# Performance work log

Hardware: AMD Instinct MI355X
Metric: run time of the kernel (lower is better)

Reference implementation:

```python
import jax, jax.numpy as jnp
import numpy as np

B, T, D, TY = 64, 512, 96, 512
H, DK = 4, 32            # num_heads, embed_dim_per_head
E = H * DK               # embed_dim = 128
P = 2                    # function='L' -> 2 coefficients
L, HID = 64, 128         # latent_dim, hidden_dim


def setup_inputs() -> dict:
    key = jax.random.key(0)
    ks = jax.random.split(key, 16)
    inp = {
        "timesteps": jax.random.uniform(ks[0], (B, T), jnp.float32),
        "X": jax.random.normal(ks[1], (B, T, D), jnp.float32),
        "M": jax.random.randint(ks[2], (B, T, D), 0, 2).astype(jnp.float32),
        "y_time_steps": jax.random.uniform(ks[3], (B, TY), jnp.float32),
        # time_embedding: Linear(1, E)
        "te_w": jax.random.normal(ks[4], (E,), jnp.float32),
        "te_b": jax.random.normal(ks[5], (E,), jnp.float32) * 0.1,
        # learned query [1, P, E]
        "query": jax.random.normal(ks[6], (1, P, E), jnp.float32),
        # query_map / key_map: Linear(E, E), stored [in, out]
        "q_w": jax.random.normal(ks[7], (E, E), jnp.float32) / np.sqrt(E),
        "q_b": jax.random.normal(ks[8], (E,), jnp.float32) * 0.1,
        "k_w": jax.random.normal(ks[9], (E, E), jnp.float32) / np.sqrt(E),
        "k_b": jax.random.normal(ks[10], (E,), jnp.float32) * 0.1,
        # attn shared out: Linear(2D*H, L)
        "ow": jax.random.normal(ks[11], (2 * D * H, L), jnp.float32) / np.sqrt(2 * D * H),
        "ob": jnp.zeros((L,), jnp.float32),
        # decoder MLP: Linear(L,HID)+ReLU+Linear(HID,D)
        "w1": jax.random.normal(ks[12], (L, HID), jnp.float32) / np.sqrt(L),
        "b1": jnp.zeros((HID,), jnp.float32),
        "w2": jax.random.normal(ks[13], (HID, D), jnp.float32) / np.sqrt(HID),
        "b2": jnp.zeros((D,), jnp.float32),
    }
    return inp


def _fld_forward(timesteps, X, M, y_time_steps, te_w, te_b, query,
                 q_w, q_b, k_w, k_b, ow, ob, w1, b1, w2, b2):
    b, t, d = X.shape
    # time embedding: Linear(1,E), sin applied to indices i % H == 0
    emb = timesteps[..., None] * te_w + te_b               # [B,T,E]
    sin_idx = (jnp.arange(E) % H) == 0
    emb = jnp.where(sin_idx, jnp.sin(emb), emb)

    X_cat = jnp.concatenate([X, M], axis=-1)               # [B,T,2D]
    M_cat = jnp.concatenate([M, M], axis=-1)               # [B,T,2D]

    q = query @ q_w + q_b                                   # [1,P,E]
    k = emb @ k_w + k_b                                     # [B,T,E]
    q = q.reshape(1, P, H, DK).transpose(0, 2, 1, 3)        # [1,H,P,dk]
    k = k.reshape(b, t, H, DK).transpose(0, 2, 1, 3)        # [B,H,T,dk]

    scores = jnp.einsum('xhpd,bhtd->bhpt', q, k) / np.sqrt(DK)  # [B,H,P,T]
    # broadcast over value feature dim, mask per-feature, softmax over T
    logits = jnp.where(M_cat[:, None, None, :, :] == 0, -jnp.inf,
                       scores[..., None])                   # [B,H,P,T,2D]
    p = jax.nn.softmax(logits, axis=-2)
    xa = jnp.einsum('bhptf,btf->bhpf', p, X_cat)            # [B,H,P,2D]
    xa = xa.transpose(0, 2, 1, 3).reshape(b, P, H * 2 * d)  # [B,P,H*2D]
    coeffs = xa @ ow + ob                                   # [B,P,L]

    # function 'L': linear in y_time_steps
    x = coeffs[:, 0][:, None, :] + y_time_steps[:, :, None] * coeffs[:, 1][:, None, :]
    h1 = jax.nn.relu(x @ w1 + b1)
    return h1 @ w2 + b2                                     # [B,TY,D]


def reference(timesteps, X, M, y_time_steps, te_w, te_b, query,
              q_w, q_b, k_w, k_b, ow, ob, w1, b1, w2, b2):
    return _fld_forward(timesteps, X, M, y_time_steps, te_w, te_b, query,
                        q_w, q_b, k_w, k_b, ow, ob, w1, b1, w2, b2)
```

## Files before the change

### kernel.cpp

```cpp
#include <hip/hip_runtime.h>
#include <math.h>

#define B_   64
#define T_   512
#define D_   96
#define TY_  512
#define H_   4
#define DK_  32
#define E_   128
#define P_   2
#define L_   64
#define HID_ 128

#define WS_OB2P  1024
#define WS_PN    2048
#define WS_PD    395264
#define WS_AB    788480

__global__ __launch_bounds__(256) void kspool(
    const float* __restrict__ tsteps, const float* __restrict__ te_w,
    const float* __restrict__ te_b,   const float* __restrict__ X,
    const float* __restrict__ M,      const float* __restrict__ query,
    const float* __restrict__ q_w,    const float* __restrict__ q_b,
    const float* __restrict__ k_w,    const float* __restrict__ k_b,
    const float* __restrict__ ow,     float* __restrict__ ws)
{
    const int c = blockIdx.x, b = blockIdx.y, tid = threadIdx.x;
    __shared__ float qm[P_ * E_];
    __shared__ float w2q_s[E_ * 8];
    __shared__ float tw_s[E_], tb_s[E_], bq_s[8];
    __shared__ float w_s[64 * 8];
    __shared__ float red[96 * 17];
    __shared__ float obp2[4][64];

    {
        int p = tid >> 7, ep = tid & 127;
        float acc = q_b[ep];
        #pragma unroll 4
        for (int e = 0; e < E_; ++e)
            acc += query[p * E_ + e] * q_w[e * E_ + ep];
        qm[p * E_ + ep] = acc;
    }
    if (tid < E_) { tw_s[tid] = te_w[tid]; tb_s[tid] = te_b[tid]; }
    __syncthreads();
    const float rs = 0.17677669529663687f;
    #pragma unroll
    for (int i = 0; i < 4; ++i) {
        int idx = tid + i * 256;
        int e = idx >> 3, hp = idx & 7, h = hp >> 1, p = hp & 1;
        float acc = 0.f;
        #pragma unroll
        for (int dk = 0; dk < DK_; ++dk)
            acc += k_w[e * E_ + h * DK_ + dk] * qm[p * E_ + h * DK_ + dk];
        w2q_s[idx] = acc * rs;
    }
    if (tid < 8) {
        int hp = tid, h = hp >> 1, p = hp & 1;
        float acc = 0.f;
        #pragma unroll
        for (int dk = 0; dk < DK_; ++dk)
            acc += k_b[h * DK_ + dk] * qm[p * E_ + h * DK_ + dk];
        bq_s[hp] = acc * rs;
    }
    __syncthreads();

    {
        const int t = tid & 63, hpg = tid >> 6, hp0 = hpg * 2;
        const float tv = tsteps[b * T_ + c * 64 + t];
        float a0 = 0.f, a1 = 0.f;
        #pragma unroll 4
        for (int e = 0; e < E_; ++e) {
            float v = tv * tw_s[e] + tb_s[e];
            if ((e & 3) == 0) v = __sinf(v);
            float2 w = *(const float2*)&w2q_s[e * 8 + hp0];
            a0 += v * w.x;
            a1 += v * w.y;
        }
        w_s[t * 8 + hp0]     = __expf(a0 + bq_s[hp0]);
        w_s[t * 8 + hp0 + 1] = __expf(a1 + bq_s[hp0 + 1]);
    }
    __syncthreads();

    const int fid = tid & 127, slice = tid >> 7;
    float num[8] = {0.f, 0.f, 0.f, 0.f, 0.f, 0.f, 0.f, 0.f};
    float den[8] = {0.f, 0.f, 0.f, 0.f, 0.f, 0.f, 0.f, 0.f};
    if (fid < 96) {
        #pragma unroll 4
        for (int i = 0; i < 32; ++i) {
            int tl = slice + 2 * i;
            size_t base = ((size_t)(b * T_ + c * 64 + tl)) * D_ + fid;
            float m = M[base], x = X[base];
            float mx = m * x;
            const float* wr = w_s + tl * 8;
            #pragma unroll
            for (int hp = 0; hp < 8; ++hp) {
                num[hp] += wr[hp] * mx;
                den[hp] += wr[hp] * m;
            }
        }
    }
    __syncthreads();
    if (slice == 1 && fid < 96) {
        #pragma unroll
        for (int hp = 0; hp < 8; ++hp) {
            red[fid * 17 + hp]     = num[hp];
            red[fid * 17 + 8 + hp] = den[hp];
        }
    }
    __syncthreads();
    if (slice == 0 && fid < 96) {
        float* pN = ws + WS_PN + ((size_t)((b * 8 + c) * 8)) * 96;
        float* pD = ws + WS_PD + ((size_t)((b * 8 + c) * 8)) * 96;
        #pragma unroll
        for (int hp = 0; hp < 8; ++hp) {
            pN[hp * 96 + fid] = num[hp] + red[fid * 17 + hp];
            pD[hp * 96 + fid] = den[hp] + red[fid * 17 + 8 + hp];
        }
    }

    if (b == 0) {
        int sub = tid >> 6, l = tid & 63;
        float acc = 0.f;
        #pragma unroll
        for (int k = 0; k < 12; ++k) {
            int hj = c * 48 + sub * 12 + k;
            int h = hj / 96, j = hj - h * 96;
            acc += ow[(size_t)(h * 2 * D_ + D_ + j) * L_ + l];
        }
        obp2[sub][l] = acc;
        __syncthreads();
        if (sub == 0)
            ws[WS_OB2P + c * 64 + l] = obp2[0][l] + obp2[1][l] + obp2[2][l] + obp2[3][l];
    }
}

__global__ __launch_bounds__(256) void kab(
    const float* __restrict__ ow, const float* __restrict__ w1,
    const float* __restrict__ b1, const float* __restrict__ ob,
    float* __restrict__ ws)
{
    const int b = blockIdx.x, tid = threadIdx.x;
    __shared__ float xa_s[8 * 96];
    __shared__ float cfp[4][2][64];
    __shared__ float cf_s[2][64];
    __shared__ float abp[2][2][128];

    for (int flat = tid; flat < 8 * 96; flat += 256) {
        int hp = flat / 96, f = flat - hp * 96;
        float n = 0.f, d = 0.f;
        #pragma unroll
        for (int c = 0; c < 8; ++c) {
            n += ws[WS_PN + ((size_t)((b * 8 + c) * 8 + hp)) * 96 + f];
            d += ws[WS_PD + ((size_t)((b * 8 + c) * 8 + hp)) * 96 + f];
        }
        xa_s[flat] = n / d;
    }
    __syncthreads();

    #pragma unroll
    for (int it = 0; it < 2; ++it) {
        int idx = tid + it * 256;
        int h = idx >> 7, p = (idx >> 6) & 1, l = idx & 63;
        const float* xr = xa_s + (h * 2 + p) * 96;
        const float* owr = ow + (size_t)(h * 2 * D_) * L_ + l;
        float acc = 0.f;
        #pragma unroll 4
        for (int f = 0; f < 96; ++f)
            acc += xr[f] * owr[(size_t)f * L_];
        cfp[h][p][l] = acc;
    }
    __syncthreads();

    if (tid < 128) {
        int p = tid >> 6, l = tid & 63;
        float v = cfp[0][p][l] + cfp[1][p][l] + cfp[2][p][l] + cfp[3][p][l] + ob[l];
        #pragma unroll
        for (int g = 0; g < 8; ++g) v += ws[WS_OB2P + g * 64 + l];
        cf_s[p][l] = v;
    }
    __syncthreads();

    {
        int s = tid >> 7, j = tid & 127;
        float a0 = 0.f, a1 = 0.f;
        #pragma unroll 4
        for (int li = 0; li < 32; ++li) {
            int l = s * 32 + li;
            float wv = w1[l * HID_ + j];
            a0 += cf_s[0][l] * wv;
            a1 += cf_s[1][l] * wv;
        }
        abp[s][0][j] = a0;
        abp[s][1][j] = a1;
    }
    __syncthreads();

    if (tid < 128) {
        ws[WS_AB + b * 256 + tid] = abp[0][0][tid] + abp[1][0][tid] + b1[tid];
    } else {
        int j = tid - 128;
        ws[WS_AB + b * 256 + 128 + j] = abp[0][1][j] + abp[1][1][j];
    }
}

__global__ __launch_bounds__(256) void kdec(
    const float* __restrict__ yts, const float* __restrict__ w2,
    const float* __restrict__ b2,  const float* __restrict__ ws,
    float* __restrict__ out)
{
    __shared__ float w2_s[HID_ * D_];
    __shared__ float a0_s[HID_], a1_s[HID_];
    __shared__ float y_s[64];
    const int tid = threadIdx.x;
    const int posb = blockIdx.x * 64;
    const int b = posb >> 9;

    {
        const float4* src = (const float4*)w2;
        float4* dst = (float4*)w2_s;
        #pragma unroll
        for (int i = 0; i < 12; ++i) dst[tid + i * 256] = src[tid + i * 256];
    }
    if (tid < 64) y_s[tid] = yts[posb + tid];
    if (tid >= 64 && tid < 192) {
        int j = tid - 64;
        a0_s[j] = ws[WS_AB + b * 256 + j];
        a1_s[j] = ws[WS_AB + b * 256 + 128 + j];
    }
    __syncthreads();

    const int pos = tid & 63, ds = tid >> 6;
    const float y = y_s[pos];
    const float* wrow = w2_s + ds * 24;

    float acc[24];
    #pragma unroll
    for (int dd = 0; dd < 24; ++dd) acc[dd] = 0.f;

    #pragma unroll 4
    for (int j = 0; j < HID_; ++j) {
        float h = fmaxf(0.f, a0_s[j] + y * a1_s[j]);
        const float* wr = wrow + j * D_;
        #pragma unroll
        for (int q = 0; q < 6; ++q) {
            float4 w4 = *(const float4*)(wr + q * 4);
            acc[q * 4 + 0] += h * w4.x;
            acc[q * 4 + 1] += h * w4.y;
            acc[q * 4 + 2] += h * w4.z;
            acc[q * 4 + 3] += h * w4.w;
        }
    }

    float* op = out + ((size_t)(posb + pos)) * D_ + ds * 24;
    const float* bp = b2 + ds * 24;
    #pragma unroll
    for (int q = 0; q < 6; ++q) {
        float4 v;
        v.x = acc[q * 4 + 0] + bp[q * 4 + 0];
        v.y = acc[q * 4 + 1] + bp[q * 4 + 1];
        v.z = acc[q * 4 + 2] + bp[q * 4 + 2];
        v.w = acc[q * 4 + 3] + bp[q * 4 + 3];
        *(float4*)(op + q * 4) = v;
    }
}

extern "C" void kernel_launch(void* const* d_in, const int* in_sizes, int n_in,
                              void* d_out, int out_size, void* d_ws, size_t ws_size,
                              hipStream_t stream)
{
    const float* timesteps = (const float*)d_in[0];
    const float* X         = (const float*)d_in[1];
    const float* M         = (const float*)d_in[2];
    const float* yts       = (const float*)d_in[3];
    const float* te_w      = (const float*)d_in[4];
    const float* te_b      = (const float*)d_in[5];
    const float* query     = (const float*)d_in[6];
    const float* q_w       = (const float*)d_in[7];
    const float* q_b       = (const float*)d_in[8];
    const float* k_w       = (const float*)d_in[9];
    const float* k_b       = (const float*)d_in[10];
    const float* ow        = (const float*)d_in[11];
    const float* ob        = (const float*)d_in[12];
    const float* w1        = (const float*)d_in[13];
    const float* b1        = (const float*)d_in[14];
    const float* w2        = (const float*)d_in[15];
    const float* b2        = (const float*)d_in[16];
    float* out = (float*)d_out;
    float* ws  = (float*)d_ws;

    kspool<<<dim3(8, B_), 256, 0, stream>>>(timesteps, te_w, te_b, X, M,
                                            query, q_w, q_b, k_w, k_b, ow, ws);
    kab<<<B_, 256, 0, stream>>>(ow, w1, b1, ob, ws);
    kdec<<<(B_ * TY_) / 64, 256, 0, stream>>>(yts, w2, b2, ws, out);
}
```

Before: 163.1 us.

## Fuse three kernels into one cooperative kernel with grid sync

Merges the pooling, coefficient and decoder kernels into a single cooperative launch of 512 blocks that synchronise across the grid between phases. A union of shared-memory layouts lets both phases reuse the same LDS. The coefficient MLP is now recomputed redundantly in each of the 512 decoder blocks instead of once per batch, and the w2 weight load is issued early into registers to overlap with that work. Falls back to two ordinary launches if the cooperative launch fails. This trades launch overhead and the intermediate round-trip for a grid barrier and duplicated small GEMMs.

```diff
diff --git a/kernel.cpp b/kernel.cpp
--- a/kernel.cpp
+++ b/kernel.cpp
@@ -1,5 +1,8 @@
 #include <hip/hip_runtime.h>
+#include <hip/hip_cooperative_groups.h>
 #include <math.h>
+
+namespace cg = cooperative_groups;
 
 #define B_   64
 #define T_   512
@@ -15,9 +18,31 @@
 #define WS_OB2P  1024
 #define WS_PN    2048
 #define WS_PD    395264
-#define WS_AB    788480
-
-__global__ __launch_bounds__(256) void kspool(
+
+struct SMemP1 {
+    float qm[P_ * E_];
+    float w2q[E_ * 8];
+    float tw[E_], tb[E_], bq[8];
+    float w[64 * 8];
+    float red[96 * 17];
+    float obp2[4][64];
+};
+struct SMemP2 {
+    float w2s[HID_ * D_];
+    float xa[8 * 96];
+    float cfp[4][2][64];
+    float cf[2][64];
+    float a0[HID_], a1[HID_];
+    float ys[64];
+    float abp[2][2][128];
+};
+union SMem {
+    SMemP1 p1;
+    SMemP2 p2;
+};
+
+__device__ __forceinline__ void phase1(
+    SMem& sm, int bi, int tid,
     const float* __restrict__ tsteps, const float* __restrict__ te_w,
     const float* __restrict__ te_b,   const float* __restrict__ X,
     const float* __restrict__ M,      const float* __restrict__ query,
@@ -25,13 +50,8 @@
     const float* __restrict__ k_w,    const float* __restrict__ k_b,
     const float* __restrict__ ow,     float* __restrict__ ws)
 {
-    const int c = blockIdx.x, b = blockIdx.y, tid = threadIdx.x;
-    __shared__ float qm[P_ * E_];
-    __shared__ float w2q_s[E_ * 8];
-    __shared__ float tw_s[E_], tb_s[E_], bq_s[8];
-    __shared__ float w_s[64 * 8];
-    __shared__ float red[96 * 17];
-    __shared__ float obp2[4][64];
+    const int c = bi & 7, b = bi >> 3;
+    SMemP1& p1 = sm.p1;
 
     {
         int p = tid >> 7, ep = tid & 127;
@@ -39,9 +59,9 @@
         #pragma unroll 4
         for (int e = 0; e < E_; ++e)
             acc += query[p * E_ + e] * q_w[e * E_ + ep];
-        qm[p * E_ + ep] = acc;
-    }
-    if (tid < E_) { tw_s[tid] = te_w[tid]; tb_s[tid] = te_b[tid]; }
+        p1.qm[p * E_ + ep] = acc;
+    }
+    if (tid < E_) { p1.tw[tid] = te_w[tid]; p1.tb[tid] = te_b[tid]; }
     __syncthreads();
     const float rs = 0.17677669529663687f;
     #pragma unroll
@@ -51,16 +71,16 @@
         float acc = 0.f;
         #pragma unroll
         for (int dk = 0; dk < DK_; ++dk)
-            acc += k_w[e * E_ + h * DK_ + dk] * qm[p * E_ + h * DK_ + dk];
-        w2q_s[idx] = acc * rs;
+            acc += k_w[e * E_ + h * DK_ + dk] * p1.qm[p * E_ + h * DK_ + dk];
+        p1.w2q[idx] = acc * rs;
     }
     if (tid < 8) {
         int hp = tid, h = hp >> 1, p = hp & 1;
         float acc = 0.f;
         #pragma unroll
         for (int dk = 0; dk < DK_; ++dk)
-            acc += k_b[h * DK_ + dk] * qm[p * E_ + h * DK_ + dk];
-        bq_s[hp] = acc * rs;
+            acc += k_b[h * DK_ + dk] * p1.qm[p * E_ + h * DK_ + dk];
+        p1.bq[hp] = acc * rs;
     }
     __syncthreads();
 
@@ -70,14 +90,14 @@
         float a0 = 0.f, a1 = 0.f;
         #pragma unroll 4
         for (int e = 0; e < E_; ++e) {
-            float v = tv * tw_s[e] + tb_s[e];
+            float v = tv * p1.tw[e] + p1.tb[e];
             if ((e & 3) == 0) v = __sinf(v);
-            float2 w = *(const float2*)&w2q_s[e * 8 + hp0];
+            float2 w = *(const float2*)&p1.w2q[e * 8 + hp0];
             a0 += v * w.x;
             a1 += v * w.y;
         }
-        w_s[t * 8 + hp0]     = __expf(a0 + bq_s[hp0]);
-        w_s[t * 8 + hp0 + 1] = __expf(a1 + bq_s[hp0 + 1]);
+        p1.w[t * 8 + hp0]     = __expf(a0 + p1.bq[hp0]);
+        p1.w[t * 8 + hp0 + 1] = __expf(a1 + p1.bq[hp0 + 1]);
     }
     __syncthreads();
 
@@ -91,7 +111,7 @@
             size_t base = ((size_t)(b * T_ + c * 64 + tl)) * D_ + fid;
             float m = M[base], x = X[base];
             float mx = m * x;
-            const float* wr = w_s + tl * 8;
+            const float* wr = p1.w + tl * 8;
             #pragma unroll
             for (int hp = 0; hp < 8; ++hp) {
                 num[hp] += wr[hp] * mx;
@@ -103,8 +123,8 @@
     if (slice == 1 && fid < 96) {
         #pragma unroll
         for (int hp = 0; hp < 8; ++hp) {
-            red[fid * 17 + hp]     = num[hp];
-            red[fid * 17 + 8 + hp] = den[hp];
+            p1.red[fid * 17 + hp]     = num[hp];
+            p1.red[fid * 17 + 8 + hp] = den[hp];
         }
     }
     __syncthreads();
@@ -113,8 +133,8 @@
         float* pD = ws + WS_PD + ((size_t)((b * 8 + c) * 8)) * 96;
         #pragma unroll
         for (int hp = 0; hp < 8; ++hp) {
-            pN[hp * 96 + fid] = num[hp] + red[fid * 17 + hp];
-            pD[hp * 96 + fid] = den[hp] + red[fid * 17 + 8 + hp];
+            pN[hp * 96 + fid] = num[hp] + p1.red[fid * 17 + hp];
+            pD[hp * 96 + fid] = den[hp] + p1.red[fid * 17 + 8 + hp];
         }
     }
 
@@ -127,33 +147,44 @@
             int h = hj / 96, j = hj - h * 96;
             acc += ow[(size_t)(h * 2 * D_ + D_ + j) * L_ + l];
         }
-        obp2[sub][l] = acc;
+        p1.obp2[sub][l] = acc;
         __syncthreads();
         if (sub == 0)
-            ws[WS_OB2P + c * 64 + l] = obp2[0][l] + obp2[1][l] + obp2[2][l] + obp2[3][l];
-    }
-}
-
-__global__ __launch_bounds__(256) void kab(
-    const float* __restrict__ ow, const float* __restrict__ w1,
-    const float* __restrict__ b1, const float* __restrict__ ob,
-    float* __restrict__ ws)
-{
-    const int b = blockIdx.x, tid = threadIdx.x;
-    __shared__ float xa_s[8 * 96];
-    __shared__ float cfp[4][2][64];
-    __shared__ float cf_s[2][64];
-    __shared__ float abp[2][2][128];
-
-    for (int flat = tid; flat < 8 * 96; flat += 256) {
+            ws[WS_OB2P + c * 64 + l] = p1.obp2[0][l] + p1.obp2[1][l]
+                                     + p1.obp2[2][l] + p1.obp2[3][l];
+    }
+}
+
+__device__ __forceinline__ void phase2(
+    SMem& sm, int bi, int tid,
+    const float* __restrict__ ow, const float* __restrict__ ob,
+    const float* __restrict__ w1, const float* __restrict__ b1,
+    const float* __restrict__ yts, const float* __restrict__ w2,
+    const float* __restrict__ b2, const float* __restrict__ ws,
+    float* __restrict__ out)
+{
+    SMemP2& p2 = sm.p2;
+    const int b = bi >> 3;
+
+    float4 wreg[12];
+    {
+        const float4* src = (const float4*)w2;
+        #pragma unroll
+        for (int i = 0; i < 12; ++i) wreg[i] = src[tid + i * 256];
+    }
+    if (tid < 64) p2.ys[tid] = yts[bi * 64 + tid];
+
+    #pragma unroll
+    for (int it = 0; it < 3; ++it) {
+        int flat = tid + it * 256;
         int hp = flat / 96, f = flat - hp * 96;
         float n = 0.f, d = 0.f;
         #pragma unroll
-        for (int c = 0; c < 8; ++c) {
-            n += ws[WS_PN + ((size_t)((b * 8 + c) * 8 + hp)) * 96 + f];
-            d += ws[WS_PD + ((size_t)((b * 8 + c) * 8 + hp)) * 96 + f];
-        }
-        xa_s[flat] = n / d;
+        for (int cc = 0; cc < 8; ++cc) {
+            n += ws[WS_PN + ((size_t)((b * 8 + cc) * 8 + hp)) * 96 + f];
+            d += ws[WS_PD + ((size_t)((b * 8 + cc) * 8 + hp)) * 96 + f];
+        }
+        p2.xa[flat] = n / d;
     }
     __syncthreads();
 
@@ -161,22 +192,23 @@
     for (int it = 0; it < 2; ++it) {
         int idx = tid + it * 256;
         int h = idx >> 7, p = (idx >> 6) & 1, l = idx & 63;
-        const float* xr = xa_s + (h * 2 + p) * 96;
+        const float* xr = p2.xa + (h * 2 + p) * 96;
         const float* owr = ow + (size_t)(h * 2 * D_) * L_ + l;
         float acc = 0.f;
         #pragma unroll 4
         for (int f = 0; f < 96; ++f)
             acc += xr[f] * owr[(size_t)f * L_];
-        cfp[h][p][l] = acc;
+        p2.cfp[h][p][l] = acc;
     }
     __syncthreads();
 
     if (tid < 128) {
         int p = tid >> 6, l = tid & 63;
-        float v = cfp[0][p][l] + cfp[1][p][l] + cfp[2][p][l] + cfp[3][p][l] + ob[l];
+        float v = p2.cfp[0][p][l] + p2.cfp[1][p][l] + p2.cfp[2][p][l]
+                + p2.cfp[3][p][l] + ob[l];
         #pragma unroll
         for (int g = 0; g < 8; ++g) v += ws[WS_OB2P + g * 64 + l];
-        cf_s[p][l] = v;
+        p2.cf[p][l] = v;
     }
     __syncthreads();
 
@@ -187,51 +219,30 @@
         for (int li = 0; li < 32; ++li) {
             int l = s * 32 + li;
             float wv = w1[l * HID_ + j];
-            a0 += cf_s[0][l] * wv;
-            a1 += cf_s[1][l] * wv;
-        }
-        abp[s][0][j] = a0;
-        abp[s][1][j] = a1;
+            a0 += p2.cf[0][l] * wv;
+            a1 += p2.cf[1][l] * wv;
+        }
+        p2.abp[s][0][j] = a0;
+        p2.abp[s][1][j] = a1;
     }
     __syncthreads();
 
     if (tid < 128) {
-        ws[WS_AB + b * 256 + tid] = abp[0][0][tid] + abp[1][0][tid] + b1[tid];
+        p2.a0[tid] = p2.abp[0][0][tid] + p2.abp[1][0][tid] + b1[tid];
     } else {
         int j = tid - 128;
-        ws[WS_AB + b * 256 + 128 + j] = abp[0][1][j] + abp[1][1][j];
-    }
-}
-
-__global__ __launch_bounds__(256) void kdec(
-    const float* __restrict__ yts, const float* __restrict__ w2,
-    const float* __restrict__ b2,  const float* __restrict__ ws,
-    float* __restrict__ out)
-{
-    __shared__ float w2_s[HID_ * D_];
-    __shared__ float a0_s[HID_], a1_s[HID_];
-    __shared__ float y_s[64];
-    const int tid = threadIdx.x;
-    const int posb = blockIdx.x * 64;
-    const int b = posb >> 9;
-
-    {
-        const float4* src = (const float4*)w2;
-        float4* dst = (float4*)w2_s;
-        #pragma unroll
-        for (int i = 0; i < 12; ++i) dst[tid + i * 256] = src[tid + i * 256];
-    }
-    if (tid < 64) y_s[tid] = yts[posb + tid];
-    if (tid >= 64 && tid < 192) {
-        int j = tid - 64;
-        a0_s[j] = ws[WS_AB + b * 256 + j];
-        a1_s[j] = ws[WS_AB + b * 256 + 128 + j];
+        p2.a1[j] = p2.abp[0][1][j] + p2.abp[1][1][j];
+    }
+    {
+        float4* dst = (float4*)p2.w2s;
+        #pragma unroll
+        for (int i = 0; i < 12; ++i) dst[tid + i * 256] = wreg[i];
     }
     __syncthreads();
 
     const int pos = tid & 63, ds = tid >> 6;
-    const float y = y_s[pos];
-    const float* wrow = w2_s + ds * 24;
+    const float y = p2.ys[pos];
+    const float* wrow = p2.w2s + ds * 24;
 
     float acc[24];
     #pragma unroll
@@ -239,7 +250,7 @@
 
     #pragma unroll 4
     for (int j = 0; j < HID_; ++j) {
-        float h = fmaxf(0.f, a0_s[j] + y * a1_s[j]);
+        float h = fmaxf(0.f, p2.a0[j] + y * p2.a1[j]);
         const float* wr = wrow + j * D_;
         #pragma unroll
         for (int q = 0; q < 6; ++q) {
@@ -251,7 +262,7 @@
         }
     }
 
-    float* op = out + ((size_t)(posb + pos)) * D_ + ds * 24;
+    float* op = out + ((size_t)(bi * 64 + pos)) * D_ + ds * 24;
     const float* bp = b2 + ds * 24;
     #pragma unroll
     for (int q = 0; q < 6; ++q) {
@@ -262,6 +273,51 @@
         v.w = acc[q * 4 + 3] + bp[q * 4 + 3];
         *(float4*)(op + q * 4) = v;
     }
+}
+
+__global__ __launch_bounds__(256) void kfused(
+    const float* __restrict__ tsteps, const float* __restrict__ te_w,
+    const float* __restrict__ te_b,   const float* __restrict__ X,
+    const float* __restrict__ M,      const float* __restrict__ query,
+    const float* __restrict__ q_w,    const float* __restrict__ q_b,
+    const float* __restrict__ k_w,    const float* __restrict__ k_b,
+    const float* __restrict__ ow,     const float* __restrict__ ob,
+    const float* __restrict__ w1,     const float* __restrict__ b1,
+    const float* __restrict__ yts,    const float* __restrict__ w2,
+    const float* __restrict__ b2,     float* __restrict__ ws,
+    float* __restrict__ out)
+{
+    __shared__ SMem sm;
+    const int bi = blockIdx.x, tid = threadIdx.x;
+    phase1(sm, bi, tid, tsteps, te_w, te_b, X, M, query,
+           q_w, q_b, k_w, k_b, ow, ws);
+    __threadfence();
+    cg::this_grid().sync();
+    phase2(sm, bi, tid, ow, ob, w1, b1, yts, w2, b2, ws, out);
+}
+
+__global__ __launch_bounds__(256) void kphase1(
+    const float* __restrict__ tsteps, const float* __restrict__ te_w,
+    const float* __restrict__ te_b,   const float* __restrict__ X,
+    const float* __restrict__ M,      const float* __restrict__ query,
+    const float* __restrict__ q_w,    const float* __restrict__ q_b,
+    const float* __restrict__ k_w,    const float* __restrict__ k_b,
+    const float* __restrict__ ow,     float* __restrict__ ws)
+{
+    __shared__ SMem sm;
+    phase1(sm, blockIdx.x, threadIdx.x, tsteps, te_w, te_b, X, M, query,
+           q_w, q_b, k_w, k_b, ow, ws);
+}
+
+__global__ __launch_bounds__(256) void kphase2(
+    const float* __restrict__ ow, const float* __restrict__ ob,
+    const float* __restrict__ w1, const float* __restrict__ b1,
+    const float* __restrict__ yts, const float* __restrict__ w2,
+    const float* __restrict__ b2, const float* __restrict__ ws,
+    float* __restrict__ out)
+{
+    __shared__ SMem sm;
+    phase2(sm, blockIdx.x, threadIdx.x, ow, ob, w1, b1, yts, w2, b2, ws, out);
 }
 
 extern "C" void kernel_launch(void* const* d_in, const int* in_sizes, int n_in,
@@ -288,8 +344,19 @@
     float* out = (float*)d_out;
     float* ws  = (float*)d_ws;
 
-    kspool<<<dim3(8, B_), 256, 0, stream>>>(timesteps, te_w, te_b, X, M,
-                                            query, q_w, q_b, k_w, k_b, ow, ws);
-    kab<<<B_, 256, 0, stream>>>(ow, w1, b1, ob, ws);
-    kdec<<<(B_ * TY_) / 64, 256, 0, stream>>>(yts, w2, b2, ws, out);
-}
+    void* args[] = {
+        (void*)&timesteps, (void*)&te_w, (void*)&te_b, (void*)&X, (void*)&M,
+        (void*)&query, (void*)&q_w, (void*)&q_b, (void*)&k_w, (void*)&k_b,
+        (void*)&ow, (void*)&ob, (void*)&w1, (void*)&b1, (void*)&yts,
+        (void*)&w2, (void*)&b2, (void*)&ws, (void*)&out
+    };
+
+    hipError_t err = hipLaunchCooperativeKernel(
+        (const void*)kfused, dim3(512), dim3(256), args, 0, stream);
+    if (err != hipSuccess) {
+        (void)hipGetLastError();
+        kphase1<<<512, 256, 0, stream>>>(timesteps, te_w, te_b, X, M, query,
+                                         q_w, q_b, k_w, k_b, ow, ws);
+        kphase2<<<512, 256, 0, stream>>>(ow, ob, w1, b1, yts, w2, b2, ws, out);
+    }
+}
```

Measured after the change: 309.3 us. 1.9x slower.

## Fuse coefficient and decoder kernels, recompute per-batch coefficients in each block

Applied to the files above, without the earlier changes.

Merges the per-batch coefficient kernel into the decoder kernel, so each of the 512 decoder blocks recomputes its batch's attention pooling reduction and MLP first-layer vectors instead of reading them from workspace. This removes one launch and the low-parallelism 64-block stage, but repeats that work eight times per batch. The w2 weights are prefetched into registers early to overlap with the coefficient computation, and the softmax-weight shared array is transposed to an [hp][t] layout.

```diff
diff --git a/kernel.cpp b/kernel.cpp
--- a/kernel.cpp
+++ b/kernel.cpp
@@ -15,9 +15,8 @@
 #define WS_OB2P  1024
 #define WS_PN    2048
 #define WS_PD    395264
-#define WS_AB    788480
-
-__global__ __launch_bounds__(256) void kspool(
+
+__global__ __launch_bounds__(256) void kphase1(
     const float* __restrict__ tsteps, const float* __restrict__ te_w,
     const float* __restrict__ te_b,   const float* __restrict__ X,
     const float* __restrict__ M,      const float* __restrict__ query,
@@ -25,11 +24,13 @@
     const float* __restrict__ k_w,    const float* __restrict__ k_b,
     const float* __restrict__ ow,     float* __restrict__ ws)
 {
-    const int c = blockIdx.x, b = blockIdx.y, tid = threadIdx.x;
+    const int bi = blockIdx.x, tid = threadIdx.x;
+    const int c = bi & 7, b = bi >> 3;
+
     __shared__ float qm[P_ * E_];
     __shared__ float w2q_s[E_ * 8];
     __shared__ float tw_s[E_], tb_s[E_], bq_s[8];
-    __shared__ float w_s[64 * 8];
+    __shared__ float w_s[8][64];
     __shared__ float red[96 * 17];
     __shared__ float obp2[4][64];
 
@@ -76,8 +77,8 @@
             a0 += v * w.x;
             a1 += v * w.y;
         }
-        w_s[t * 8 + hp0]     = __expf(a0 + bq_s[hp0]);
-        w_s[t * 8 + hp0 + 1] = __expf(a1 + bq_s[hp0 + 1]);
+        w_s[hp0][t]     = __expf(a0 + bq_s[hp0]);
+        w_s[hp0 + 1][t] = __expf(a1 + bq_s[hp0 + 1]);
     }
     __syncthreads();
 
@@ -91,11 +92,10 @@
             size_t base = ((size_t)(b * T_ + c * 64 + tl)) * D_ + fid;
             float m = M[base], x = X[base];
             float mx = m * x;
-            const float* wr = w_s + tl * 8;
             #pragma unroll
             for (int hp = 0; hp < 8; ++hp) {
-                num[hp] += wr[hp] * mx;
-                den[hp] += wr[hp] * m;
+                num[hp] += w_s[hp][tl] * mx;
+                den[hp] += w_s[hp][tl] * m;
             }
         }
     }
@@ -130,28 +130,46 @@
         obp2[sub][l] = acc;
         __syncthreads();
         if (sub == 0)
-            ws[WS_OB2P + c * 64 + l] = obp2[0][l] + obp2[1][l] + obp2[2][l] + obp2[3][l];
+            ws[WS_OB2P + c * 64 + l] = obp2[0][l] + obp2[1][l]
+                                     + obp2[2][l] + obp2[3][l];
     }
 }
 
-__global__ __launch_bounds__(256) void kab(
-    const float* __restrict__ ow, const float* __restrict__ w1,
-    const float* __restrict__ b1, const float* __restrict__ ob,
-    float* __restrict__ ws)
+__global__ __launch_bounds__(256) void kphase2(
+    const float* __restrict__ ow, const float* __restrict__ ob,
+    const float* __restrict__ w1, const float* __restrict__ b1,
+    const float* __restrict__ yts, const float* __restrict__ w2,
+    const float* __restrict__ b2, const float* __restrict__ ws,
+    float* __restrict__ out)
 {
-    const int b = blockIdx.x, tid = threadIdx.x;
+    __shared__ float w2_s[HID_ * D_];
     __shared__ float xa_s[8 * 96];
     __shared__ float cfp[4][2][64];
     __shared__ float cf_s[2][64];
+    __shared__ float a0_s[HID_], a1_s[HID_];
+    __shared__ float y_s[64];
     __shared__ float abp[2][2][128];
 
-    for (int flat = tid; flat < 8 * 96; flat += 256) {
+    const int bi = blockIdx.x, tid = threadIdx.x;
+    const int b = bi >> 3;
+
+    float4 wreg[12];
+    {
+        const float4* src = (const float4*)w2;
+        #pragma unroll
+        for (int i = 0; i < 12; ++i) wreg[i] = src[tid + i * 256];
+    }
+    if (tid < 64) y_s[tid] = yts[bi * 64 + tid];
+
+    #pragma unroll
+    for (int it = 0; it < 3; ++it) {
+        int flat = tid + it * 256;
         int hp = flat / 96, f = flat - hp * 96;
         float n = 0.f, d = 0.f;
         #pragma unroll
-        for (int c = 0; c < 8; ++c) {
-            n += ws[WS_PN + ((size_t)((b * 8 + c) * 8 + hp)) * 96 + f];
-            d += ws[WS_PD + ((size_t)((b * 8 + c) * 8 + hp)) * 96 + f];
+        for (int cc = 0; cc < 8; ++cc) {
+            n += ws[WS_PN + ((size_t)((b * 8 + cc) * 8 + hp)) * 96 + f];
+            d += ws[WS_PD + ((size_t)((b * 8 + cc) * 8 + hp)) * 96 + f];
         }
         xa_s[flat] = n / d;
     }
@@ -173,7 +191,8 @@
 
     if (tid < 128) {
         int p = tid >> 6, l = tid & 63;
-        float v = cfp[0][p][l] + cfp[1][p][l] + cfp[2][p][l] + cfp[3][p][l] + ob[l];
+        float v = cfp[0][p][l] + cfp[1][p][l] + cfp[2][p][l]
+                + cfp[3][p][l] + ob[l];
         #pragma unroll
         for (int g = 0; g < 8; ++g) v += ws[WS_OB2P + g * 64 + l];
         cf_s[p][l] = v;
@@ -196,36 +215,15 @@
     __syncthreads();
 
     if (tid < 128) {
-        ws[WS_AB + b * 256 + tid] = abp[0][0][tid] + abp[1][0][tid] + b1[tid];
+        a0_s[tid] = abp[0][0][tid] + abp[1][0][tid] + b1[tid];
     } else {
         int j = tid - 128;
-        ws[WS_AB + b * 256 + 128 + j] = abp[0][1][j] + abp[1][1][j];
-    }
-}
-
-__global__ __launch_bounds__(256) void kdec(
-    const float* __restrict__ yts, const float* __restrict__ w2,
-    const float* __restrict__ b2,  const float* __restrict__ ws,
-    float* __restrict__ out)
-{
-    __shared__ float w2_s[HID_ * D_];
-    __shared__ float a0_s[HID_], a1_s[HID_];
-    __shared__ float y_s[64];
-    const int tid = threadIdx.x;
-    const int posb = blockIdx.x * 64;
-    const int b = posb >> 9;
-
-    {
-        const float4* src = (const float4*)w2;
+        a1_s[j] = abp[0][1][j] + abp[1][1][j];
+    }
+    {
         float4* dst = (float4*)w2_s;
         #pragma unroll
-        for (int i = 0; i < 12; ++i) dst[tid + i * 256] = src[tid + i * 256];
-    }
-    if (tid < 64) y_s[tid] = yts[posb + tid];
-    if (tid >= 64 && tid < 192) {
-        int j = tid - 64;
-        a0_s[j] = ws[WS_AB + b * 256 + j];
-        a1_s[j] = ws[WS_AB + b * 256 + 128 + j];
+        for (int i = 0; i < 12; ++i) dst[tid + i * 256] = wreg[i];
     }
     __syncthreads();
 
@@ -251,7 +249,7 @@
         }
     }
 
-    float* op = out + ((size_t)(posb + pos)) * D_ + ds * 24;
+    float* op = out + ((size_t)(bi * 64 + pos)) * D_ + ds * 24;
     const float* bp = b2 + ds * 24;
     #pragma unroll
     for (int q = 0; q < 6; ++q) {
@@ -288,8 +286,7 @@
     float* out = (float*)d_out;
     float* ws  = (float*)d_ws;
 
-    kspool<<<dim3(8, B_), 256, 0, stream>>>(timesteps, te_w, te_b, X, M,
-                                            query, q_w, q_b, k_w, k_b, ow, ws);
-    kab<<<B_, 256, 0, stream>>>(ow, w1, b1, ob, ws);
-    kdec<<<(B_ * TY_) / 64, 256, 0, stream>>>(yts, w2, b2, ws, out);
+    kphase1<<<512, 256, 0, stream>>>(timesteps, te_w, te_b, X, M, query,
+                                     q_w, q_b, k_w, k_b, ow, ws);
+    kphase2<<<512, 256, 0, stream>>>(ow, ob, w1, b1, yts, w2, b2, ws, out);
 }
```

Result: slower. 168.6 us (+3.3%).
